# Performance work log

Measured on AMD Instinct MI355X. Metric: run time of the kernel, lower is better.

Reference implementation:

```python
import jax, jax.numpy as jnp
import numpy as np

L, B, S, H, NH, F = 4, 2, 1024, 1024, 16, 4096
DH = H // NH

def setup_inputs() -> dict:
    key = jax.random.key(0)
    ks = jax.random.split(key, 16)
    std = 0.02
    return {
        'x': jax.random.normal(ks[0], (B, S, H), jnp.float32),
        'attention_mask': jnp.ones((B, S, S), jnp.float32),
        'wq': jax.random.normal(ks[1], (L, H, H), jnp.float32) * std,
        'bq': jnp.zeros((L, H), jnp.float32),
        'wk': jax.random.normal(ks[2], (L, H, H), jnp.float32) * std,
        'bk': jnp.zeros((L, H), jnp.float32),
        'wv': jax.random.normal(ks[3], (L, H, H), jnp.float32) * std,
        'bv': jnp.zeros((L, H), jnp.float32),
        'wo_attn': jax.random.normal(ks[4], (L, H, H), jnp.float32) * std,
        'bo_attn': jnp.zeros((L, H), jnp.float32),
        'alpha_attn': jax.random.uniform(ks[5], (L,), jnp.float32) * 0.1,
        'wi': jax.random.normal(ks[6], (L, H, F), jnp.float32) * std,
        'bi': jnp.zeros((L, F), jnp.float32),
        'wo_ffn': jax.random.normal(ks[7], (L, F, H), jnp.float32) * std,
        'bo_ffn': jnp.zeros((L, H), jnp.float32),
        'alpha_ffn': jax.random.uniform(ks[8], (L,), jnp.float32) * 0.1,
    }

def _heads(t):
    # [B,S,H] -> [B,NH,S,DH]
    return t.reshape(B, S, NH, DH).transpose(0, 2, 1, 3)

def reference(x, attention_mask, wq, bq, wk, bk, wv, bv, wo_attn, bo_attn,
              alpha_attn, wi, bi, wo_ffn, bo_ffn, alpha_ffn):
    # additive mask: (1 - mask) * -10000, broadcast over heads
    adder = (1.0 - attention_mask)[:, None, :, :] * -10000.0  # [B,1,S,S]
    scale = 1.0 / jnp.sqrt(jnp.asarray(DH, x.dtype))
    for l in range(L):
        q = _heads(x @ wq[l] + bq[l])
        k = _heads(x @ wk[l] + bk[l])
        v = _heads(x @ wv[l] + bv[l])
        scores = jnp.einsum('bhqd,bhkd->bhqk', q, k) * scale + adder
        probs = jax.nn.softmax(scores, axis=-1)
        ctx = jnp.einsum('bhqk,bhkd->bhqd', probs, v)
        ctx = ctx.transpose(0, 2, 1, 3).reshape(B, S, H)
        attn_out = ctx @ wo_attn[l] + bo_attn[l]
        x = x + alpha_attn[l] * attn_out  # rezero residual
        inter = jax.nn.gelu(x @ wi[l] + bi[l], approximate=True)
        ffn_out = inter @ wo_ffn[l] + bo_ffn[l]
        x = x + alpha_ffn[l] * ffn_out  # rezero residual
    return x
```

## Files before the change

kernel.cpp:

```cpp
#include <hip/hip_runtime.h>
#include <cstdint>

#define B_  2
#define S_  1024
#define H_  1024
#define NH_ 16
#define DH_ 64
#define F_  4096
#define L_  4
#define M_  (B_*S_)

typedef __bf16 bf16;
typedef __bf16 bf16x8 __attribute__((ext_vector_type(8)));
typedef __bf16 bf16x4 __attribute__((ext_vector_type(4)));
typedef __bf16 bf16x2 __attribute__((ext_vector_type(2)));
typedef float  f32x4  __attribute__((ext_vector_type(4)));

__device__ __forceinline__ void async_ld16(void* lds, const void* g) {
  auto* lp = reinterpret_cast<__attribute__((address_space(3))) unsigned int*>(
      reinterpret_cast<uintptr_t>(lds));
  const auto* gp = reinterpret_cast<const __attribute__((address_space(1))) unsigned int*>(
      reinterpret_cast<uintptr_t>(g));
  __builtin_amdgcn_global_load_lds(gp, lp, 16, 0, 0);
}

__device__ __forceinline__ float gelu_tanh(float x) {
  float u = 0.7978845608028654f * (x + 0.044715f * x * x * x);
  u = fminf(fmaxf(u, -15.f), 15.f);
  float e = __builtin_amdgcn_exp2f(u * 2.8853900817779268f);
  return 0.5f * x * (1.f + (e - 1.f) / (e + 1.f));
}

__global__ __launch_bounds__(256) void transpose_all(
    const float* __restrict__ wq, const float* __restrict__ wk,
    const float* __restrict__ wv, const float* __restrict__ wo,
    const float* __restrict__ wi, const float* __restrict__ wf,
    bf16* __restrict__ WtQKV, bf16* __restrict__ WtO,
    bf16* __restrict__ WtI, bf16* __restrict__ WtF) {
  const size_t HH = (size_t)H_ * H_;
  const size_t HF = (size_t)H_ * F_;
  int idx = blockIdx.x;
  const float* src;
  bf16* dst;
  int N, K, kk0, n0;
  if (idx < 1024) {
    const int mat = idx >> 6;
    const int s = mat >> 2, l = mat & 3;
    const int t = idx & 63;
    kk0 = (t >> 5) * 512; n0 = (t & 31) * 32;
    N = H_; K = H_;
    src = (s == 0 ? wq : s == 1 ? wk : s == 2 ? wv : wo) + (size_t)l * HH;
    dst = (s < 3) ? (WtQKV + (size_t)l * 3 * HH + (size_t)s * HH)
                  : (WtO + (size_t)l * HH);
  } else if (idx < 2048) {
    const int j = idx - 1024;
    const int l = j >> 8;
    const int t = j & 255;
    kk0 = (t >> 7) * 512; n0 = (t & 127) * 32;
    N = F_; K = H_;
    src = wi + (size_t)l * HF;
    dst = WtI + (size_t)l * HF;
  } else {
    const int j = idx - 2048;
    const int l = j >> 8;
    const int t = j & 255;
    kk0 = (t >> 5) * 512; n0 = (t & 31) * 32;
    N = H_; K = F_;
    src = wf + (size_t)l * HF;
    dst = WtF + (size_t)l * HF;
  }
  __shared__ __align__(16) bf16 t[32][520];
  const int tid = (int)threadIdx.x;
  const int r = tid >> 3, c = tid & 7;
  #pragma unroll
  for (int p = 0; p < 16; ++p) {
    const int k = p * 32 + r;
    const float4 v = *(const float4*)(src + (size_t)(kk0 + k) * N + n0 + c * 4);
    t[c * 4 + 0][k] = (bf16)v.x;
    t[c * 4 + 1][k] = (bf16)v.y;
    t[c * 4 + 2][k] = (bf16)v.z;
    t[c * 4 + 3][k] = (bf16)v.w;
  }
  __syncthreads();
  const int ln = tid & 63, wv_ = tid >> 6;
  #pragma unroll
  for (int p = 0; p < 8; ++p) {
    const int n = p * 4 + wv_;
    *(bf16x8*)(dst + (size_t)(n0 + n) * K + kk0 + ln * 8) =
        *(const bf16x8*)&t[n][ln * 8];
  }
}

__global__ __launch_bounds__(256) void prep_kernel(
    const float4* __restrict__ mask, bf16x4* __restrict__ madd,
    const float4* __restrict__ x, float4* __restrict__ xf,
    bf16x4* __restrict__ xb) {
  const int blk = blockIdx.x;
  if (blk < 2048) {
    const int i = blk * 256 + (int)threadIdx.x;
    const float c2 = -10000.f * 1.44269504088896f;
    float4 v = mask[i];
    bf16x4 o;
    o[0] = (bf16)((1.f - v.x) * c2);
    o[1] = (bf16)((1.f - v.y) * c2);
    o[2] = (bf16)((1.f - v.z) * c2);
    o[3] = (bf16)((1.f - v.w) * c2);
    madd[i] = o;
  } else {
    const int i = (blk - 2048) * 256 + (int)threadIdx.x;
    float4 v = x[i];
    xf[i] = v;
    bf16x4 b;
    b[0] = (bf16)v.x; b[1] = (bf16)v.y; b[2] = (bf16)v.z; b[3] = (bf16)v.w;
    xb[i] = b;
  }
}

__device__ __forceinline__ void gemm_core(
    const bf16* __restrict__ A, const bf16* __restrict__ Bt, int ld, int kLen,
    int m0, int n0, bf16* As, bf16* Bs, f32x4 (&acc)[4][4]) {
  const int tid = (int)threadIdx.x;
  const int w = tid >> 6, l = tid & 63;
  const int lr = l & 15, lg = l >> 4;
  const int wm = w >> 1, wn = w & 1;
  const int srow = l >> 2;
  const int scol = (l & 3) * 8;

  const bf16* ag = A  + (size_t)(m0 + w * 32 + srow) * ld + scol;
  const bf16* bg = Bt + (size_t)(n0 + w * 32 + srow) * ld + scol;
  const int soff = (w * 32) * 32;

  auto stage = [&](int buf, int kk) {
    bf16* ad = As + buf * 4096 + soff;
    bf16* bd = Bs + buf * 4096 + soff;
    async_ld16(ad,           ag + kk);
    async_ld16(ad + 16 * 32, ag + kk + (size_t)16 * ld);
    async_ld16(bd,           bg + kk);
    async_ld16(bd + 16 * 32, bg + kk + (size_t)16 * ld);
  };

  stage(0, 0);
  __syncthreads();
  int cur = 0;
  for (int k0 = 0; k0 < kLen; k0 += 32) {
    if (k0 + 32 < kLen) stage(cur ^ 1, k0 + 32);
    const bf16* Ab = As + cur * 4096;
    const bf16* Bb = Bs + cur * 4096;
    bf16x8 af[4], bv[4];
    #pragma unroll
    for (int i = 0; i < 4; ++i)
      af[i] = *(const bf16x8*)(Ab + (wm * 64 + i * 16 + lr) * 32 + lg * 8);
    #pragma unroll
    for (int i = 0; i < 4; ++i)
      bv[i] = *(const bf16x8*)(Bb + (wn * 64 + i * 16 + lr) * 32 + lg * 8);
    #pragma unroll
    for (int i = 0; i < 4; ++i)
      #pragma unroll
      for (int j = 0; j < 4; ++j)
        acc[i][j] = __builtin_amdgcn_mfma_f32_16x16x32_bf16(af[i], bv[j], acc[i][j], 0, 0, 0);
    __syncthreads();
    cur ^= 1;
  }
}

template <int MODE>
__global__ __launch_bounds__(256) void gemm128_kernel(
    const bf16* __restrict__ A, const bf16* __restrict__ Bt,
    const float* __restrict__ bias, bf16* __restrict__ outb,
    int N, int K, int kSlice) {
  __shared__ __align__(16) bf16 As[2 * 128 * 32];
  __shared__ __align__(16) bf16 Bs[2 * 128 * 32];
  const int m0 = blockIdx.y * 128, n0 = blockIdx.x * 128;
  const int z = blockIdx.z;
  const f32x4 z4 = {0.f, 0.f, 0.f, 0.f};
  f32x4 acc[4][4];
  #pragma unroll
  for (int i = 0; i < 4; ++i)
    #pragma unroll
    for (int j = 0; j < 4; ++j) acc[i][j] = z4;

  gemm_core(A + (size_t)z * kSlice, Bt + (size_t)z * kSlice, K, kSlice,
            m0, n0, As, Bs, acc);

  const int tid = (int)threadIdx.x;
  const int w = tid >> 6, l = tid & 63;
  const int lr = l & 15, lg = l >> 4;
  const int wm = w >> 1, wn = w & 1;
  const size_t pbase = (MODE == 3) ? (size_t)z * M_ * (size_t)N : 0;
  #pragma unroll
  for (int i = 0; i < 4; ++i) {
    const int row0 = m0 + wm * 64 + i * 16 + lg * 4;
    #pragma unroll
    for (int j = 0; j < 4; ++j) {
      const int col = n0 + wn * 64 + j * 16 + lr;
      const float bvx = (MODE == 3) ? 0.f : bias[col];
      #pragma unroll
      for (int r = 0; r < 4; ++r) {
        const size_t idx = (size_t)(row0 + r) * N + col;
        float v = acc[i][j][r] + bvx;
        if (MODE == 3) {
          outb[pbase + idx] = (bf16)v;
        } else {
          outb[idx] = (bf16)gelu_tanh(v);
        }
      }
    }
  }
}

__global__ __launch_bounds__(256) void reduce_residual(
    const bf16x4* __restrict__ part, const float* __restrict__ bias,
    const float* __restrict__ alphap, float4* __restrict__ xf,
    bf16x4* __restrict__ xb) {
  const int i = blockIdx.x * 256 + (int)threadIdx.x;
  const int nper = M_ * H_ / 4;
  float s[4] = {0.f, 0.f, 0.f, 0.f};
  #pragma unroll
  for (int zz = 0; zz < 4; ++zz) {
    const bf16x4 p = part[i + (size_t)zz * nper];
    #pragma unroll
    for (int k = 0; k < 4; ++k) s[k] += (float)p[k];
  }
  const int col = (i * 4) & (H_ - 1);
  const float4 b4 = *(const float4*)(bias + col);
  const float a = *alphap;
  float4 xv = xf[i];
  xv.x += a * (s[0] + b4.x);
  xv.y += a * (s[1] + b4.y);
  xv.z += a * (s[2] + b4.z);
  xv.w += a * (s[3] + b4.w);
  xf[i] = xv;
  bf16x4 bb;
  bb[0] = (bf16)xv.x; bb[1] = (bf16)xv.y; bb[2] = (bf16)xv.z; bb[3] = (bf16)xv.w;
  xb[i] = bb;
}

__global__ __launch_bounds__(256) void gemm_qkv64(
    const bf16* __restrict__ A, const bf16* __restrict__ Wt,
    const float* __restrict__ bq, const float* __restrict__ bk,
    const float* __restrict__ bvv,
    bf16* __restrict__ qo, bf16* __restrict__ ko, bf16* __restrict__ vt) {
  __shared__ __align__(16) bf16 As[2 * 128 * 32];
  __shared__ __align__(16) bf16 Bs[2 * 64 * 32];
  const int tid = (int)threadIdx.x;
  const int w = tid >> 6, l = tid & 63;
  const int lr = l & 15, lg = l >> 4;
  const int wm = w >> 1, wn = w & 1;
  const int srow = l >> 2, scol = (l & 3) * 8;
  const int m0 = blockIdx.y * 128, n0 = blockIdx.x * 64;

  const bf16* ag = A  + (size_t)(m0 + w * 32 + srow) * H_ + scol;
  const bf16* bg = Wt + (size_t)(n0 + w * 16 + srow) * H_ + scol;
  const int aoff = (w * 32) * 32;
  const int boff = (w * 16) * 32;

  auto stage = [&](int buf, int kk) {
    bf16* ad = As + buf * 4096 + aoff;
    bf16* bd = Bs + buf * 2048 + boff;
    async_ld16(ad,           ag + kk);
    async_ld16(ad + 16 * 32, ag + kk + (size_t)16 * H_);
    async_ld16(bd,           bg + kk);
  };

  const f32x4 z4 = {0.f, 0.f, 0.f, 0.f};
  f32x4 acc[4][2];
  #pragma unroll
  for (int i = 0; i < 4; ++i)
    #pragma unroll
    for (int j = 0; j < 2; ++j) acc[i][j] = z4;

  stage(0, 0);
  __syncthreads();
  int cur = 0;
  for (int k0 = 0; k0 < H_; k0 += 32) {
    if (k0 + 32 < H_) stage(cur ^ 1, k0 + 32);
    const bf16* Ab = As + cur * 4096;
    const bf16* Bb = Bs + cur * 2048;
    bf16x8 af[4], bv[2];
    #pragma unroll
    for (int i = 0; i < 4; ++i)
      af[i] = *(const bf16x8*)(Ab + (wm * 64 + i * 16 + lr) * 32 + lg * 8);
    #pragma unroll
    for (int j = 0; j < 2; ++j)
      bv[j] = *(const bf16x8*)(Bb + (wn * 32 + j * 16 + lr) * 32 + lg * 8);
    #pragma unroll
    for (int i = 0; i < 4; ++i)
      #pragma unroll
      for (int j = 0; j < 2; ++j)
        acc[i][j] = __builtin_amdgcn_mfma_f32_16x16x32_bf16(af[i], bv[j], acc[i][j], 0, 0, 0);
    __syncthreads();
    cur ^= 1;
  }

  if (n0 < 2048) {
    bf16* out = (n0 < 1024) ? qo : ko;
    const float* bias = (n0 < 1024) ? bq : bk;
    const int nl = n0 & 1023;
    #pragma unroll
    for (int i = 0; i < 4; ++i) {
      const int row0 = m0 + wm * 64 + i * 16 + lg * 4;
      #pragma unroll
      for (int j = 0; j < 2; ++j) {
        const int col = nl + wn * 32 + j * 16 + lr;
        const float bvx = bias[col];
        #pragma unroll
        for (int r = 0; r < 4; ++r)
          out[(size_t)(row0 + r) * H_ + col] = (bf16)(acc[i][j][r] + bvx);
      }
    }
  } else {
    const int hh = (n0 >> 6) - 32;
    #pragma unroll
    for (int i = 0; i < 4; ++i) {
      const int row0 = m0 + wm * 64 + i * 16 + lg * 4;
      const int bb = row0 >> 10, ss = row0 & (S_ - 1);
      #pragma unroll
      for (int j = 0; j < 2; ++j) {
        const int dd = wn * 32 + j * 16 + lr;
        const float bvx = bvv[hh * 64 + dd];
        bf16x4 pk;
        #pragma unroll
        for (int r = 0; r < 4; ++r) pk[r] = (bf16)(acc[i][j][r] + bvx);
        *(bf16x4*)(vt + (((size_t)(bb * NH_ + hh) * DH_ + dd) << 10) + ss) = pk;
      }
    }
  }
}

__global__ __launch_bounds__(256) void attn_kernel7(
    const bf16* __restrict__ Q, const bf16* __restrict__ Kb,
    const bf16* __restrict__ Vt, const bf16* __restrict__ madd,
    bf16* __restrict__ Ctx) {
  const int tid = (int)threadIdx.x;
  const int w = tid >> 6, l = tid & 63;
  const int lr = l & 15, lg = l >> 4;
  const int r7 = lr & 7;
  const int h = blockIdx.y, b = blockIdx.z;
  const int q0 = blockIdx.x * 64 + w * 16;

  __shared__ __align__(16) bf16 Kt[2][64 * 64];
  __shared__ __align__(16) bf16 Vs[2][64 * 64];
  __shared__ unsigned int Pu[4][16][36];

  const bf16* qp = Q + ((size_t)(b * S_ + q0 + lr)) * H_ + h * DH_;
  const bf16x8 qa0 = *(const bf16x8*)(qp + lg * 8);
  const bf16x8 qa1 = *(const bf16x8*)(qp + 32 + lg * 8);

  const f32x4 z4 = {0.f, 0.f, 0.f, 0.f};
  f32x4 acc[4];
  #pragma unroll
  for (int dt = 0; dt < 4; ++dt) acc[dt] = z4;
  float mrow = -1e30f, ssum = 0.f;

  const bf16* Kbase = Kb + ((size_t)b * S_) * H_ + h * DH_;
  const bf16* Vbase = Vt + ((size_t)(b * NH_ + h)) * DH_ * S_;
  const bf16* Mb = madd + ((size_t)(b * S_ + q0 + lr)) * S_;

  const float c1 = 0.125f * 1.44269504088896f;
  const float THR = 10.f;

  const int sub = l >> 3;
  const int cs  = ((l & 7) ^ sub) * 8;
  auto stage = [&](int buf, int kv) {
    #pragma unroll
    for (int j = 0; j < 2; ++j) {
      const int rbase = w * 16 + j * 8;
      async_ld16(&Kt[buf][rbase * 64],
                 Kbase + (size_t)(kv + rbase + sub) * H_ + cs);
      async_ld16(&Vs[buf][rbase * 64],
                 Vbase + (size_t)(rbase + sub) * S_ + kv + cs);
    }
  };

  stage(0, 0);
  bf16x4 mk[4];
  #pragma unroll
  for (int t = 0; t < 4; ++t) mk[t] = *(const bf16x4*)(Mb + t * 16 + lg * 4);
  __syncthreads();
  int cur = 0;
  #pragma unroll 1
  for (int it = 0; it < 16; ++it) {
    const int kv0 = it * 64;
    if (it < 15) stage(cur ^ 1, kv0 + 64);
    bf16x4 mkn[4];
    if (it < 15) {
      #pragma unroll
      for (int t = 0; t < 4; ++t)
        mkn[t] = *(const bf16x4*)(Mb + kv0 + 64 + t * 16 + lg * 4);
    }
    const bf16* Kc = &Kt[cur][0];
    const bf16* Vc = &Vs[cur][0];
    bf16x8 kf0[4], kf1[4];
    #pragma unroll
    for (int t = 0; t < 4; ++t) {
      kf0[t] = *(const bf16x8*)(Kc + (t * 16 + lr) * 64 + ((lg ^ r7) * 8));
      kf1[t] = *(const bf16x8*)(Kc + (t * 16 + lr) * 64 + (((4 + lg) ^ r7) * 8));
    }
    f32x4 st[4];
    __builtin_amdgcn_s_setprio(1);
    #pragma unroll
    for (int t = 0; t < 4; ++t) {
      f32x4 s = __builtin_amdgcn_mfma_f32_16x16x32_bf16(kf0[t], qa0, z4, 0, 0, 0);
      st[t] = __builtin_amdgcn_mfma_f32_16x16x32_bf16(kf1[t], qa1, s, 0, 0, 0);
    }
    __builtin_amdgcn_s_setprio(0);
    float sv[4][4];
    #pragma unroll
    for (int t = 0; t < 4; ++t)
      #pragma unroll
      for (int r = 0; r < 4; ++r)
        sv[t][r] = st[t][r] * c1 + (float)mk[t][r];
    float nm = sv[0][0];
    #pragma unroll
    for (int t = 0; t < 4; ++t)
      #pragma unroll
      for (int r = 0; r < 4; ++r) nm = fmaxf(nm, sv[t][r]);
    nm = fmaxf(nm, __shfl_xor(nm, 16));
    nm = fmaxf(nm, __shfl_xor(nm, 32));
    if (__any(nm > mrow + THR)) {
      float newm = fmaxf(mrow, nm);
      float f = __builtin_amdgcn_exp2f(mrow - newm);
      mrow = newm;
      ssum *= f;
      #pragma unroll
      for (int dt = 0; dt < 4; ++dt)
        #pragma unroll
        for (int r = 0; r < 4; ++r) acc[dt][r] *= f;
    }
    float p[4][4];
    float ps = 0.f;
    #pragma unroll
    for (int t = 0; t < 4; ++t)
      #pragma unroll
      for (int r = 0; r < 4; ++r) {
        p[t][r] = __builtin_amdgcn_exp2f(sv[t][r] - mrow);
        ps += p[t][r];
      }
    ps += __shfl_xor(ps, 16);
    ps += __shfl_xor(ps, 32);
    ssum += ps;
    #pragma unroll
    for (int t = 0; t < 4; ++t)
      #pragma unroll
      for (int hh = 0; hh < 2; ++hh) {
        union { bf16x2 v; unsigned int u; } pk;
        pk.v[0] = (bf16)p[t][2 * hh];
        pk.v[1] = (bf16)p[t][2 * hh + 1];
        Pu[w][lr][8 * t + 2 * lg + hh] = pk.u;
      }
    const bf16x8 pf0 = *(const bf16x8*)&Pu[w][lr][4 * lg];
    const bf16x8 pf1 = *(const bf16x8*)&Pu[w][lr][16 + 4 * lg];
    __builtin_amdgcn_s_setprio(1);
    #pragma unroll
    for (int dt = 0; dt < 4; ++dt) {
      bf16x8 vb0 = *(const bf16x8*)(Vc + (dt * 16 + lr) * 64 + ((lg ^ r7) * 8));
      acc[dt] = __builtin_amdgcn_mfma_f32_16x16x32_bf16(vb0, pf0, acc[dt], 0, 0, 0);
    }
    #pragma unroll
    for (int dt = 0; dt < 4; ++dt) {
      bf16x8 vb1 = *(const bf16x8*)(Vc + (dt * 16 + lr) * 64 + (((4 + lg) ^ r7) * 8));
      acc[dt] = __builtin_amdgcn_mfma_f32_16x16x32_bf16(vb1, pf1, acc[dt], 0, 0, 0);
    }
    __builtin_amdgcn_s_setprio(0);
    if (it < 15) {
      #pragma unroll
      for (int t = 0; t < 4; ++t) mk[t] = mkn[t];
    }
    __syncthreads();
    cur ^= 1;
  }
  const float inv = 1.f / ssum;
  bf16* cp = Ctx + ((size_t)(b * S_ + q0 + lr)) * H_ + h * DH_;
  #pragma unroll
  for (int dt = 0; dt < 4; ++dt) {
    bf16x4 o;
    #pragma unroll
    for (int r = 0; r < 4; ++r) o[r] = (bf16)(acc[dt][r] * inv);
    *(bf16x4*)(cp + dt * 16 + lg * 4) = o;
  }
}

extern "C" void kernel_launch(void* const* d_in, const int* in_sizes, int n_in,
                              void* d_out, int out_size, void* d_ws, size_t ws_size,
                              hipStream_t stream) {
  (void)in_sizes; (void)n_in; (void)out_size; (void)ws_size;
  const float* x    = (const float*)d_in[0];
  const float* mask = (const float*)d_in[1];
  const float* wq   = (const float*)d_in[2];
  const float* bq   = (const float*)d_in[3];
  const float* wk   = (const float*)d_in[4];
  const float* bk   = (const float*)d_in[5];
  const float* wv   = (const float*)d_in[6];
  const float* bv   = (const float*)d_in[7];
  const float* wo   = (const float*)d_in[8];
  const float* bo   = (const float*)d_in[9];
  const float* aat  = (const float*)d_in[10];
  const float* wi   = (const float*)d_in[11];
  const float* bi   = (const float*)d_in[12];
  const float* wf   = (const float*)d_in[13];
  const float* bf_  = (const float*)d_in[14];
  const float* afn  = (const float*)d_in[15];

  char* ws = (char*)d_ws;
  size_t o = 0;
  bf16* WtQKV = (bf16*)(ws + o); o += (size_t)L_ * 3 * H_ * H_ * 2;
  bf16* WtO = (bf16*)(ws + o); o += (size_t)L_ * H_ * H_ * 2;
  bf16* WtI = (bf16*)(ws + o); o += (size_t)L_ * H_ * F_ * 2;
  bf16* WtF = (bf16*)(ws + o); o += (size_t)L_ * F_ * H_ * 2;
  bf16* madd = (bf16*)(ws + o); o += (size_t)B_ * S_ * S_ * 2;
  bf16* xb  = (bf16*)(ws + o); o += (size_t)M_ * H_ * 2;
  bf16* qb  = (bf16*)(ws + o); o += (size_t)M_ * H_ * 2;
  bf16* kbf = (bf16*)(ws + o); o += (size_t)M_ * H_ * 2;
  bf16* vt  = (bf16*)(ws + o); o += (size_t)M_ * H_ * 2;
  bf16* ctx = (bf16*)(ws + o); o += (size_t)M_ * H_ * 2;
  bf16* itm = (bf16*)(ws + o); o += (size_t)M_ * F_ * 2;
  bf16* partb = (bf16*)(ws + o); o += (size_t)4 * M_ * H_ * 2;

  float* xf = (float*)d_out;

  const size_t HH = (size_t)H_ * H_;
  transpose_all<<<dim3(3072), 256, 0, stream>>>(
      wq, wk, wv, wo, wi, wf, WtQKV, WtO, WtI, WtF);
  prep_kernel<<<dim3(4096), 256, 0, stream>>>(
      (const float4*)mask, (bf16x4*)madd, (const float4*)x, (float4*)xf,
      (bf16x4*)xb);

  for (int l = 0; l < L_; ++l) {
    gemm_qkv64<<<dim3(48, M_/128), 256, 0, stream>>>(
        xb, WtQKV + (size_t)l * 3 * HH,
        bq + l * H_, bk + l * H_, bv + l * H_, qb, kbf, vt);
    attn_kernel7<<<dim3(S_/64, NH_, B_), 256, 0, stream>>>(
        qb, kbf, vt, madd, ctx);
    gemm128_kernel<3><<<dim3(H_/128, M_/128, 4), 256, 0, stream>>>(
        ctx, WtO + (size_t)l * HH, nullptr, partb, H_, H_, H_ / 4);
    reduce_residual<<<dim3((M_ * H_ / 4) / 256), 256, 0, stream>>>(
        (const bf16x4*)partb, bo + l * H_, aat + l, (float4*)xf, (bf16x4*)xb);
    gemm128_kernel<1><<<dim3(F_/128, M_/128), 256, 0, stream>>>(
        xb, WtI + (size_t)l * H_ * F_, bi + l * F_, itm, F_, H_, H_);
    gemm128_kernel<3><<<dim3(H_/128, M_/128, 4), 256, 0, stream>>>(
        itm, WtF + (size_t)l * F_ * H_, nullptr, partb, H_, F_, F_ / 4);
    reduce_residual<<<dim3((M_ * H_ / 4) / 256), 256, 0, stream>>>(
        (const bf16x4*)partb, bf_ + l * H_, afn + l, (float4*)xf, (bf16x4*)xb);
  }
}
```

Baseline: 603.0 us.

## Merge weight transpose and input prep into one kernel with async LDS loads

The weight-transpose and mask/x preparation kernels are combined into a single launch, removing one kernel launch and its tail. The transpose switches from 32x512 tiles converted on load to 128x128 fp32 tiles brought in with global_load_lds async copies, and conversion to bf16 happens when reading LDS. The 64KB LDS tile lowers occupancy, and the strided column reads from LDS may cause bank conflicts.

```diff
diff --git a/kernel.cpp b/kernel.cpp
--- a/kernel.cpp
+++ b/kernel.cpp
@@ -31,23 +31,50 @@
   return 0.5f * x * (1.f + (e - 1.f) / (e + 1.f));
 }
 
-__global__ __launch_bounds__(256) void transpose_all(
+__global__ __launch_bounds__(256) void prep_all(
     const float* __restrict__ wq, const float* __restrict__ wk,
     const float* __restrict__ wv, const float* __restrict__ wo,
     const float* __restrict__ wi, const float* __restrict__ wf,
     bf16* __restrict__ WtQKV, bf16* __restrict__ WtO,
-    bf16* __restrict__ WtI, bf16* __restrict__ WtF) {
+    bf16* __restrict__ WtI, bf16* __restrict__ WtF,
+    const float4* __restrict__ mask, bf16x4* __restrict__ madd,
+    const float4* __restrict__ x, float4* __restrict__ xf,
+    bf16x4* __restrict__ xb) {
+  __shared__ __align__(16) float t[128 * 128];
+  const int tid = (int)threadIdx.x;
+  int idx = blockIdx.x;
+  if (idx >= 3072) {
+    idx -= 3072;
+    if (idx < 2048) {
+      const int i = idx * 256 + tid;
+      const float c2 = -10000.f * 1.44269504088896f;
+      float4 v = mask[i];
+      bf16x4 o;
+      o[0] = (bf16)((1.f - v.x) * c2);
+      o[1] = (bf16)((1.f - v.y) * c2);
+      o[2] = (bf16)((1.f - v.z) * c2);
+      o[3] = (bf16)((1.f - v.w) * c2);
+      madd[i] = o;
+    } else {
+      const int i = (idx - 2048) * 256 + tid;
+      float4 v = x[i];
+      xf[i] = v;
+      bf16x4 b;
+      b[0] = (bf16)v.x; b[1] = (bf16)v.y; b[2] = (bf16)v.z; b[3] = (bf16)v.w;
+      xb[i] = b;
+    }
+    return;
+  }
   const size_t HH = (size_t)H_ * H_;
   const size_t HF = (size_t)H_ * F_;
-  int idx = blockIdx.x;
   const float* src;
   bf16* dst;
   int N, K, kk0, n0;
   if (idx < 1024) {
     const int mat = idx >> 6;
     const int s = mat >> 2, l = mat & 3;
-    const int t = idx & 63;
-    kk0 = (t >> 5) * 512; n0 = (t & 31) * 32;
+    const int tt = idx & 63;
+    kk0 = (tt >> 3) * 128; n0 = (tt & 7) * 128;
     N = H_; K = H_;
     src = (s == 0 ? wq : s == 1 ? wk : s == 2 ? wv : wo) + (size_t)l * HH;
     dst = (s < 3) ? (WtQKV + (size_t)l * 3 * HH + (size_t)s * HH)
@@ -55,64 +82,36 @@
   } else if (idx < 2048) {
     const int j = idx - 1024;
     const int l = j >> 8;
-    const int t = j & 255;
-    kk0 = (t >> 7) * 512; n0 = (t & 127) * 32;
+    const int tt = j & 255;
+    kk0 = (tt >> 5) * 128; n0 = (tt & 31) * 128;
     N = F_; K = H_;
     src = wi + (size_t)l * HF;
     dst = WtI + (size_t)l * HF;
   } else {
     const int j = idx - 2048;
     const int l = j >> 8;
-    const int t = j & 255;
-    kk0 = (t >> 5) * 512; n0 = (t & 31) * 32;
+    const int tt = j & 255;
+    kk0 = (tt >> 3) * 128; n0 = (tt & 7) * 128;
     N = H_; K = F_;
     src = wf + (size_t)l * HF;
     dst = WtF + (size_t)l * HF;
   }
-  __shared__ __align__(16) bf16 t[32][520];
-  const int tid = (int)threadIdx.x;
-  const int r = tid >> 3, c = tid & 7;
-  #pragma unroll
-  for (int p = 0; p < 16; ++p) {
-    const int k = p * 32 + r;
-    const float4 v = *(const float4*)(src + (size_t)(kk0 + k) * N + n0 + c * 4);
-    t[c * 4 + 0][k] = (bf16)v.x;
-    t[c * 4 + 1][k] = (bf16)v.y;
-    t[c * 4 + 2][k] = (bf16)v.z;
-    t[c * 4 + 3][k] = (bf16)v.w;
+  const int w = tid >> 6, li = tid & 63;
+  #pragma unroll
+  for (int q = 0; q < 16; ++q) {
+    const int r2 = 2 * (q * 4 + w);
+    async_ld16(&t[r2 * 128],
+               src + (size_t)(kk0 + r2 + (li >> 5)) * N + n0 + (li & 31) * 4);
   }
   __syncthreads();
-  const int ln = tid & 63, wv_ = tid >> 6;
   #pragma unroll
   for (int p = 0; p < 8; ++p) {
-    const int n = p * 4 + wv_;
-    *(bf16x8*)(dst + (size_t)(n0 + n) * K + kk0 + ln * 8) =
-        *(const bf16x8*)&t[n][ln * 8];
-  }
-}
-
-__global__ __launch_bounds__(256) void prep_kernel(
-    const float4* __restrict__ mask, bf16x4* __restrict__ madd,
-    const float4* __restrict__ x, float4* __restrict__ xf,
-    bf16x4* __restrict__ xb) {
-  const int blk = blockIdx.x;
-  if (blk < 2048) {
-    const int i = blk * 256 + (int)threadIdx.x;
-    const float c2 = -10000.f * 1.44269504088896f;
-    float4 v = mask[i];
-    bf16x4 o;
-    o[0] = (bf16)((1.f - v.x) * c2);
-    o[1] = (bf16)((1.f - v.y) * c2);
-    o[2] = (bf16)((1.f - v.z) * c2);
-    o[3] = (bf16)((1.f - v.w) * c2);
-    madd[i] = o;
-  } else {
-    const int i = (blk - 2048) * 256 + (int)threadIdx.x;
-    float4 v = x[i];
-    xf[i] = v;
-    bf16x4 b;
-    b[0] = (bf16)v.x; b[1] = (bf16)v.y; b[2] = (bf16)v.z; b[3] = (bf16)v.w;
-    xb[i] = b;
+    const int n = p * 16 + (tid >> 4);
+    const int k0 = (tid & 15) * 8;
+    bf16x8 pk;
+    #pragma unroll
+    for (int j = 0; j < 8; ++j) pk[j] = (bf16)t[(k0 + j) * 128 + n];
+    *(bf16x8*)(dst + (size_t)(n0 + n) * K + kk0 + k0) = pk;
   }
 }
 
@@ -519,9 +518,8 @@
   float* xf = (float*)d_out;
 
   const size_t HH = (size_t)H_ * H_;
-  transpose_all<<<dim3(3072), 256, 0, stream>>>(
-      wq, wk, wv, wo, wi, wf, WtQKV, WtO, WtI, WtF);
-  prep_kernel<<<dim3(4096), 256, 0, stream>>>(
+  prep_all<<<dim3(7168), 256, 0, stream>>>(
+      wq, wk, wv, wo, wi, wf, WtQKV, WtO, WtI, WtF,
       (const float4*)mask, (bf16x4*)madd, (const float4*)x, (float4*)xf,
       (bf16x4*)xb);
 
```

Measured after the change: 603.7 us (median of 3 runs). No clear change (+0.1%).
